# Performance work log

Measured on AMD Instinct MI355X. Metric: run time of the kernel, lower is better.

Reference implementation:

```python
import jax, jax.numpy as jnp
import numpy as np

N = 100000   # nodes of target type
N1 = 80000   # nodes of second type
D = 128      # raw feature dim
H = 64       # hidden dim
C = 16       # n_classes
G = 3        # number of graphs (metapaths)
E = 1000000  # edges per graph
K = 20       # neighbors per node for NS branch
LP_LAYERS = 3


def setup_inputs() -> dict:
    key = jax.random.key(0)
    ks = jax.random.split(key, 24)
    f = lambda i, shape: jax.random.normal(ks[i], shape, dtype=jnp.float32)
    feats0 = f(0, (N, D))
    feats1 = f(1, (N1, D))
    W0 = f(2, (D, H)) * 0.05
    b0 = jnp.zeros((H,), jnp.float32)
    W1 = f(3, (D, H)) * 0.05
    b1 = jnp.zeros((H,), jnp.float32)
    Wp = f(4, (D, H)) * 0.05
    Wcls = f(5, (H, C)) * 0.05
    bcls = jnp.zeros((C,), jnp.float32)
    alpha = f(6, (N, 1)) * 0.1
    attention = f(7, (N, G, 1))
    y = jax.random.randint(ks[8], (N,), 0, C)
    labels_one_hot = jax.nn.one_hot(y, C, dtype=jnp.float32)
    byte_idx_train = jax.random.bernoulli(ks[9], 0.3, (N, 1))
    label_init = jnp.full((N, C), 1.0 / C, jnp.float32)
    nei_idx = jax.random.randint(ks[10], (N, K), 0, N1, dtype=jnp.int32)
    src0 = jax.random.randint(ks[11], (E,), 0, N, dtype=jnp.int32)
    dst0 = jax.random.randint(ks[12], (E,), 0, N, dtype=jnp.int32)
    src1 = jax.random.randint(ks[13], (E,), 0, N, dtype=jnp.int32)
    dst1 = jax.random.randint(ks[14], (E,), 0, N, dtype=jnp.int32)
    src2 = jax.random.randint(ks[15], (E,), 0, N, dtype=jnp.int32)
    dst2 = jax.random.randint(ks[16], (E,), 0, N, dtype=jnp.int32)
    return dict(feats0=feats0, feats1=feats1, W0=W0, b0=b0, W1=W1, b1=b1,
                Wp=Wp, Wcls=Wcls, bcls=bcls, alpha=alpha, attention=attention,
                labels_one_hot=labels_one_hot, label_init=label_init,
                byte_idx_train=byte_idx_train, nei_idx=nei_idx,
                src0=src0, dst0=dst0, src1=src1, dst1=dst1, src2=src2, dst2=dst2)


def _propagate(fp, h, src, dst, n):
    # edge attention: dot-product score of projected feats, softmax per dst
    s = jnp.sum(fp[src] * fp[dst], axis=-1) / np.sqrt(fp.shape[-1])   # [E]
    m = jax.ops.segment_max(s, dst, num_segments=n)                   # [N]
    e = jnp.exp(s - jnp.where(jnp.isfinite(m), m, 0.0)[dst])          # [E]
    denom = jax.ops.segment_sum(e, dst, num_segments=n)               # [N]
    att = e / (denom[dst] + 1e-16)                                    # [E]
    return jax.ops.segment_sum(att[:, None] * h[src], dst, num_segments=n)


def reference(feats0, feats1, W0, b0, W1, b1, Wp, Wcls, bcls, alpha, attention,
              labels_one_hot, label_init, byte_idx_train, nei_idx,
              src0, dst0, src1, dst1, src2, dst2):
    n = label_init.shape[0]
    masked = byte_idx_train.astype(jnp.float32)          # [N,1]
    masked_label = 1.0 - masked                          # (~mask).float()
    masked_onehot = labels_one_hot * masked              # clamp train labels

    fp = feats0 @ Wp                                     # shared projected feats [N,H]
    h_prime = []
    for src, dst in ((src0, dst0), (src1, dst1), (src2, dst2)):
        h = label_init
        for _ in range(LP_LAYERS):
            h = _propagate(fp, h, src, dst, n)
            h = h * masked_label + masked_onehot
        h_prime.append(h)
    x = jnp.stack(h_prime, axis=-1)                      # [N, C, G]
    att_g = jax.nn.softmax(attention, axis=1)            # [N, G, 1]
    logits_lp = jnp.matmul(x, att_g).squeeze(-1)         # [N, C]

    # NS_ec branch: per-type projection + neighbor-mean aggregation + classifier
    h0 = feats0 @ W0 + b0                                # [N, H]
    h1 = feats1 @ W1 + b1                                # [N1, H]
    z = h0 + jnp.mean(h1[nei_idx], axis=1)               # [N, H]
    logits_ns = z @ Wcls + bcls                          # [N, C]

    gate = jax.nn.sigmoid(alpha)
    logits = gate * logits_lp + jax.nn.sigmoid(-alpha) * logits_ns
    return logits, logits_lp, logits_ns
```

## Files before the change

### kernel.cpp

```cpp
#include <hip/hip_runtime.h>
#include <stdint.h>
#include <stddef.h>

__device__ __forceinline__ float bl(unsigned u){ return __uint_as_float(u << 16); }
__device__ __forceinline__ float bh(unsigned u){ return __uint_as_float(u & 0xffff0000u); }
__device__ __forceinline__ unsigned short f2bf(float f){
    unsigned u = __float_as_uint(f);
    unsigned r = (u + 0x7fffu + ((u >> 16) & 1u)) >> 16;
    return (unsigned short)r;
}
__device__ __forceinline__ void ntstore_u2(uint2* p, unsigned x, unsigned y){
    unsigned long long v = ((unsigned long long)y << 32) | (unsigned long long)x;
    __builtin_nontemporal_store(v, (unsigned long long*)p);
}
__device__ __forceinline__ float get_mask(const void* p, unsigned flags, int i){
    if((flags & 1u) == 0) return ((const int*)p)[i] ? 1.0f : 0.0f;
    if(flags & 2u)        return ((const float*)p)[i];
    return ((const unsigned char*)p)[i] ? 1.0f : 0.0f;
}

__global__ __launch_bounds__(256) void prep_kernel(
    const float* __restrict__ W0, const float* __restrict__ b0,
    const float* __restrict__ W1, const float* __restrict__ b1,
    const float* __restrict__ Wcls, const float* __restrict__ bcls,
    float* __restrict__ W0c, float* __restrict__ W1c,
    float* __restrict__ b0c, float* __restrict__ b1c,
    const unsigned char* __restrict__ mp, int n,
    const unsigned* __restrict__ li, long li_n, unsigned* __restrict__ flags,
    int* __restrict__ deg, int n3)
{
    int t = threadIdx.x;
    if(blockIdx.x == 0){
        for(int i = t; i < 2048; i += 256){
            int d = i >> 4, c = i & 15;
            float s0 = 0.f, s1 = 0.f;
            for(int k = 0; k < 64; k++){
                float wc = Wcls[k*16 + c];
                s0 += W0[d*64 + k]*wc;
                s1 += W1[d*64 + k]*wc;
            }
            W0c[i] = s0; W1c[i] = s1;
        }
        if(t < 16){
            float s0 = 0.f, s1 = 0.f;
            for(int k = 0; k < 64; k++){
                float wc = Wcls[k*16 + t];
                s0 += b0[k]*wc; s1 += b1[k]*wc;
            }
            b0c[t] = s0 + bcls[t];
            b1c[t] = s1;
        }
    } else {
        long i = (long)(blockIdx.x - 1)*256 + t;
        if(i < n3) deg[i] = 0;
        unsigned f = 0;
        if(i < n){
            unsigned char b = mp[i];
            if((i & 3) && b) f |= 1u;
            if(b == 0x3Fu)   f |= 2u;
        }
        if(i < li_n){
            if(li[i] != li[0]) f |= 4u;
        }
        if(f) atomicOr(flags, f);
    }
}

__global__ __launch_bounds__(256) void proj_fused0(
    const float* __restrict__ X, const float* __restrict__ Wp,
    const float* __restrict__ W0c, const float* __restrict__ b0c,
    unsigned short* __restrict__ fph, float* __restrict__ h0c, int rows)
{
    __shared__ float Wl[128*64];
    __shared__ float Wcl[128*16];
    __shared__ float ftile[32*128];
    int t = threadIdx.x;
    for(int i = t; i < 2048; i += 256) ((float4*)Wl)[i]  = ((const float4*)Wp)[i];
    for(int i = t; i < 512;  i += 256) ((float4*)Wcl)[i] = ((const float4*)W0c)[i];
    int c4 = (t & 15)*4;
    int col16 = t & 15;
    int r2 = (t >> 4)*2;
    float bc = b0c[col16];
    for(long base = (long)blockIdx.x*32; base < rows; base += (long)gridDim.x*32){
        int nr = min(32, (int)(rows - base));
        __syncthreads();
        for(int i = t; i < nr*32; i += 256){
            int r = i >> 5, q = i & 31;
            ((float4*)ftile)[r*32 + q] = ((const float4*)X)[(base + r)*32 + q];
        }
        __syncthreads();
        float a00=0,a01=0,a02=0,a03=0, a10=0,a11=0,a12=0,a13=0;
        float c0 = bc, c1 = bc;
        #pragma unroll 4
        for(int k = 0; k < 128; k++){
            float4 w = *((const float4*)(Wl + k*64 + c4));
            float wc = Wcl[k*16 + col16];
            float x0 = ftile[r2*128 + k];
            float x1 = ftile[(r2+1)*128 + k];
            a00 += x0*w.x; a01 += x0*w.y; a02 += x0*w.z; a03 += x0*w.w; c0 += x0*wc;
            a10 += x1*w.x; a11 += x1*w.y; a12 += x1*w.z; a13 += x1*w.w; c1 += x1*wc;
        }
        if(r2 < nr){
            ushort4 o; o.x=f2bf(a00); o.y=f2bf(a01); o.z=f2bf(a02); o.w=f2bf(a03);
            *((ushort4*)(fph + (base + r2)*64 + c4)) = o;
            h0c[(base + r2)*16 + col16] = c0;
        }
        if(r2 + 1 < nr){
            ushort4 o; o.x=f2bf(a10); o.y=f2bf(a11); o.z=f2bf(a12); o.w=f2bf(a13);
            *((ushort4*)(fph + (base + r2 + 1)*64 + c4)) = o;
            h0c[(base + r2 + 1)*16 + col16] = c1;
        }
    }
}

__global__ __launch_bounds__(256) void proj16_count_kernel(
    const float* __restrict__ X, const float* __restrict__ Wc,
    const float* __restrict__ biasc, unsigned short* __restrict__ Y, int rows,
    int nbProj,
    const int* __restrict__ dst0, const int* __restrict__ dst1, const int* __restrict__ dst2,
    int* __restrict__ deg, int n, int eg)
{
    __shared__ float Wcl[128*16];
    __shared__ float ftile[64*128];
    int t = threadIdx.x;
    if(blockIdx.x < nbProj){
        for(int i = t; i < 512; i += 256) ((float4*)Wcl)[i] = ((const float4*)Wc)[i];
        int col = t & 15;
        int r4 = (t >> 4)*4;
        float bc = biasc[col];
        long base = (long)blockIdx.x*64;
        if(base < rows){
            int nr = min(64, (int)(rows - base));
            __syncthreads();
            for(int i = t; i < nr*32; i += 256){
                int r = i >> 5, q = i & 31;
                ((float4*)ftile)[r*32 + q] = ((const float4*)X)[(base + r)*32 + q];
            }
            __syncthreads();
            float acc0 = bc, acc1 = bc, acc2 = bc, acc3 = bc;
            #pragma unroll 4
            for(int k = 0; k < 128; k++){
                float wc = Wcl[k*16 + col];
                acc0 += ftile[(r4+0)*128 + k]*wc;
                acc1 += ftile[(r4+1)*128 + k]*wc;
                acc2 += ftile[(r4+2)*128 + k]*wc;
                acc3 += ftile[(r4+3)*128 + k]*wc;
            }
            if(r4+0 < nr) Y[(base + r4 + 0)*16 + col] = f2bf(acc0);
            if(r4+1 < nr) Y[(base + r4 + 1)*16 + col] = f2bf(acc1);
            if(r4+2 < nr) Y[(base + r4 + 2)*16 + col] = f2bf(acc2);
            if(r4+3 < nr) Y[(base + r4 + 3)*16 + col] = f2bf(acc3);
        }
    } else {
        long tid = (long)(blockIdx.x - nbProj)*256 + t;
        if(tid < 3L*eg){
            int g = (int)(tid / eg);
            int e = (int)(tid - (long)g*eg);
            const int* dp = g==0 ? dst0 : (g==1 ? dst1 : dst2);
            atomicAdd(&deg[(long)g*n + dp[e]], 1);
        }
    }
}

__global__ __launch_bounds__(256) void scanA_kernel(const int* __restrict__ deg,
                                                    int* __restrict__ incl,
                                                    int* __restrict__ bsum, int n3)
{
    __shared__ int sh[256];
    int t = threadIdx.x;
    long base = (long)blockIdx.x*1024 + t*4;
    int v0=0,v1=0,v2=0,v3=0;
    if(base   < n3) v0 = deg[base];
    if(base+1 < n3) v1 = deg[base+1];
    if(base+2 < n3) v2 = deg[base+2];
    if(base+3 < n3) v3 = deg[base+3];
    int tot = v0+v1+v2+v3;
    sh[t] = tot;
    __syncthreads();
    for(int ofs = 1; ofs < 256; ofs <<= 1){
        int add = (t >= ofs) ? sh[t-ofs] : 0;
        __syncthreads();
        sh[t] += add;
        __syncthreads();
    }
    int pre = sh[t] - tot;
    if(t == 255) bsum[blockIdx.x] = sh[255];
    int s0 = pre+v0, s1 = s0+v1, s2 = s1+v2, s3 = s2+v3;
    if(base   < n3) incl[base]   = s0;
    if(base+1 < n3) incl[base+1] = s1;
    if(base+2 < n3) incl[base+2] = s2;
    if(base+3 < n3) incl[base+3] = s3;
}

__global__ __launch_bounds__(512) void scanB_kernel(int* __restrict__ bsum, int nb)
{
    __shared__ int sh[512];
    int t = threadIdx.x;
    int v = (t < nb) ? bsum[t] : 0;
    sh[t] = v;
    __syncthreads();
    for(int ofs = 1; ofs < 512; ofs <<= 1){
        int add = (t >= ofs) ? sh[t-ofs] : 0;
        __syncthreads();
        sh[t] += add;
        __syncthreads();
    }
    if(t < nb) bsum[t] = sh[t] - v;
}

__global__ __launch_bounds__(256) void scanC_kernel(
    const int* __restrict__ incl, const int* __restrict__ boff,
    int* __restrict__ rowptr, int* __restrict__ cursor, int n3,
    const float* __restrict__ label_init, const float* __restrict__ labels,
    const void* __restrict__ maskp, const unsigned* __restrict__ flags,
    unsigned short* __restrict__ hA, int n)
{
    int i = blockIdx.x*blockDim.x + threadIdx.x;
    if(i >= n3) return;
    int ex = (i == 0) ? 0 : (incl[i-1] + boff[(i-1) >> 10]);
    int en = incl[i] + boff[i >> 10];
    rowptr[i] = ex;
    cursor[i] = ex;
    if(i == n3-1) rowptr[n3] = en;
    unsigned fl = *flags;
    if(!(fl & 4u)){
        int g = i / n;
        int d = i - g*n;
        float mk = get_mask(maskp, fl, d);
        float v = (en > ex) ? label_init[0]*(1.0f - mk) : 0.0f;
        const float4* lb = (const float4*)(labels + (long)d*16);
        ushort4* op = (ushort4*)(hA + (long)i*16);
        #pragma unroll
        for(int q = 0; q < 4; q++){
            float4 l4 = lb[q];
            ushort4 o;
            o.x = f2bf(v + l4.x*mk);
            o.y = f2bf(v + l4.y*mk);
            o.z = f2bf(v + l4.z*mk);
            o.w = f2bf(v + l4.w*mk);
            op[q] = o;
        }
    }
}

__global__ __launch_bounds__(256) void score_scatter_packed(
    const unsigned short* __restrict__ fph,
    const int* __restrict__ src0, const int* __restrict__ dst0,
    const int* __restrict__ src1, const int* __restrict__ dst1,
    const int* __restrict__ src2, const int* __restrict__ dst2,
    int* __restrict__ cursor, uint2* __restrict__ rec, int n, int eg)
{
    long tid = (long)blockIdx.x*blockDim.x + threadIdx.x;
    long gid = tid >> 3;
    long tot = 3L*eg;
    long e0 = gid*4;
    if(e0 >= tot) return;
    int l = threadIdx.x & 7;
    const uint4* f4 = (const uint4*)fph;

    int sv[4], dv[4], gv[4];
    bool ok[4];
    #pragma unroll
    for(int q = 0; q < 4; q++){
        long e = e0 + q;
        ok[q] = (e < tot);
        long ee = ok[q] ? e : (tot - 1);
        int g = (int)(ee / eg);
        int i = (int)(ee - (long)g*eg);
        const int* sp = g==0 ? src0 : (g==1 ? src1 : src2);
        const int* dp = g==0 ? dst0 : (g==1 ? dst1 : dst2);
        sv[q] = sp[i];
        dv[q] = dp[i];
        gv[q] = g;
    }
    uint4 A[4], B[4];
    #pragma unroll
    for(int q = 0; q < 4; q++){
        A[q] = f4[(long)sv[q]*8 + l];
        B[q] = f4[(long)dv[q]*8 + l];
    }
    float p[4];
    #pragma unroll
    for(int q = 0; q < 4; q++){
        float v;
        v  = bl(A[q].x)*bl(B[q].x) + bh(A[q].x)*bh(B[q].x);
        v += bl(A[q].y)*bl(B[q].y) + bh(A[q].y)*bh(B[q].y);
        v += bl(A[q].z)*bl(B[q].z) + bh(A[q].z)*bh(B[q].z);
        v += bl(A[q].w)*bl(B[q].w) + bh(A[q].w)*bh(B[q].w);
        p[q] = v;
    }
    #pragma unroll
    for(int q = 0; q < 4; q++){
        p[q] += __shfl_xor(p[q], 1);
        p[q] += __shfl_xor(p[q], 2);
        p[q] += __shfl_xor(p[q], 4);
    }
    if(l == 0){
        int pos[4];
        #pragma unroll
        for(int q = 0; q < 4; q++){
            if(ok[q]) pos[q] = atomicAdd(&cursor[(long)gv[q]*n + dv[q]], 1);
        }
        #pragma unroll
        for(int q = 0; q < 4; q++){
            if(ok[q]){
                float ev = __expf(fminf(p[q]*0.125f, 70.0f));
                ntstore_u2(&rec[pos[q]], (unsigned)sv[q], __float_as_uint(ev));
            }
        }
    }
}

__device__ __forceinline__ void prop_row_bf16(
    const uint2* __restrict__ rec, int beg, int end,
    const unsigned short* __restrict__ hg, int c4,
    float &a0, float &a1, float &a2, float &a3)
{
    float den = 0.f;
    a0 = a1 = a2 = a3 = 0.f;
    int j = beg;
    if((j & 1) && j < end){
        uint2 r = rec[j];
        float e = __uint_as_float(r.y);
        den += e;
        uint2 hv = *((const uint2*)(hg + (long)r.x*16 + c4));
        a0 += e*bl(hv.x); a1 += e*bh(hv.x); a2 += e*bl(hv.y); a3 += e*bh(hv.y);
        j++;
    }
    for(; j + 1 < end; j += 2){
        uint4 rr = *((const uint4*)(&rec[j]));
        float e0 = __uint_as_float(rr.y);
        float e1 = __uint_as_float(rr.w);
        den += e0 + e1;
        uint2 hv0 = *((const uint2*)(hg + (long)rr.x*16 + c4));
        uint2 hv1 = *((const uint2*)(hg + (long)rr.z*16 + c4));
        a0 += e0*bl(hv0.x) + e1*bl(hv1.x);
        a1 += e0*bh(hv0.x) + e1*bh(hv1.x);
        a2 += e0*bl(hv0.y) + e1*bl(hv1.y);
        a3 += e0*bh(hv0.y) + e1*bh(hv1.y);
    }
    if(j < end){
        uint2 r = rec[j];
        float e = __uint_as_float(r.y);
        den += e;
        uint2 hv = *((const uint2*)(hg + (long)r.x*16 + c4));
        a0 += e*bl(hv.x); a1 += e*bh(hv.x); a2 += e*bl(hv.y); a3 += e*bh(hv.y);
    }
    float inv = 1.0f/(den + 1e-16f);
    a0 *= inv; a1 *= inv; a2 *= inv; a3 *= inv;
}

__global__ __launch_bounds__(256) void prop1_fallback_kernel(
    const int* __restrict__ rowptr, const uint2* __restrict__ rec,
    const float* __restrict__ h_in_f32, unsigned short* __restrict__ h_next,
    const float* __restrict__ labels, const void* __restrict__ maskp,
    const unsigned* __restrict__ flags, int n)
{
    unsigned fl = *flags;
    if(!(fl & 4u)) return;
    long tid = (long)blockIdx.x*blockDim.x + threadIdx.x;
    int row = (int)(tid >> 2);
    int c4 = (int)(tid & 3)*4;
    if(row >= 3*n) return;
    int g = row / n;
    int d = row - g*n;
    int beg = rowptr[row], end = rowptr[row+1];
    float a0=0.f, a1=0.f, a2=0.f, a3=0.f, den=0.f;
    for(int j = beg; j < end; j++){
        uint2 r = rec[j];
        float e = __uint_as_float(r.y);
        den += e;
        float4 hv = *((const float4*)(h_in_f32 + (long)r.x*16 + c4));
        a0 += e*hv.x; a1 += e*hv.y; a2 += e*hv.z; a3 += e*hv.w;
    }
    float inv = 1.0f/(den + 1e-16f);
    float mk = get_mask(maskp, fl, d);
    float im = (1.0f - mk)*inv;
    float4 lb = *((const float4*)(labels + (long)d*16 + c4));
    ushort4 o;
    o.x = f2bf(a0*im + lb.x*mk);
    o.y = f2bf(a1*im + lb.y*mk);
    o.z = f2bf(a2*im + lb.z*mk);
    o.w = f2bf(a3*im + lb.w*mk);
    *((ushort4*)(h_next + (long)row*16 + c4)) = o;
}

__global__ __launch_bounds__(256) void prop_mid_kernel(
    const int* __restrict__ rowptr, const uint2* __restrict__ rec,
    const unsigned short* __restrict__ h_in, unsigned short* __restrict__ h_next,
    const float* __restrict__ labels, const void* __restrict__ maskp,
    const unsigned* __restrict__ flags, int n)
{
    long tid = (long)blockIdx.x*blockDim.x + threadIdx.x;
    int row = (int)(tid >> 2);
    int c4 = (int)(tid & 3)*4;
    if(row >= 3*n) return;
    int g = row / n;
    int d = row - g*n;
    float a0, a1, a2, a3;
    prop_row_bf16(rec, rowptr[row], rowptr[row+1], h_in + (long)g*n*16, c4,
                  a0, a1, a2, a3);
    unsigned fl = *flags;
    float mk = get_mask(maskp, fl, d);
    float im = 1.0f - mk;
    float4 lb = *((const float4*)(labels + (long)d*16 + c4));
    ushort4 o;
    o.x = f2bf(a0*im + lb.x*mk);
    o.y = f2bf(a1*im + lb.y*mk);
    o.z = f2bf(a2*im + lb.z*mk);
    o.w = f2bf(a3*im + lb.w*mk);
    *((ushort4*)(h_next + (long)row*16 + c4)) = o;
}

__global__ __launch_bounds__(256) void prop3_ns_kernel(
    const int* __restrict__ rowptr, const uint2* __restrict__ rec,
    const unsigned short* __restrict__ h_in, const float* __restrict__ labels,
    const void* __restrict__ maskp, const unsigned* __restrict__ flags,
    const float* __restrict__ h0c, const unsigned short* __restrict__ h1c,
    const int* __restrict__ nei, const float* __restrict__ attn,
    const float* __restrict__ alpha, float* __restrict__ out, int n, int kk)
{
    long tid = (long)blockIdx.x*blockDim.x + threadIdx.x;
    int node = (int)(tid >> 2);
    int c4 = (int)(tid & 3)*4;
    if(node >= n) return;
    unsigned fl = *flags;
    float mk = get_mask(maskp, fl, node);
    float im = 1.0f - mk;
    float4 lb = *((const float4*)(labels + (long)node*16 + c4));

    float lp_[3][4];
    #pragma unroll
    for(int g = 0; g < 3; g++){
        int row = g*n + node;
        float a0, a1, a2, a3;
        prop_row_bf16(rec, rowptr[row], rowptr[row+1], h_in + (long)g*n*16, c4,
                      a0, a1, a2, a3);
        lp_[g][0] = a0*im + lb.x*mk;
        lp_[g][1] = a1*im + lb.y*mk;
        lp_[g][2] = a2*im + lb.z*mk;
        lp_[g][3] = a3*im + lb.w*mk;
    }
    float t0 = attn[node*3], t1 = attn[node*3+1], t2 = attn[node*3+2];
    float mx = fmaxf(t0, fmaxf(t1, t2));
    float e0 = __expf(t0-mx), e1 = __expf(t1-mx), e2 = __expf(t2-mx);
    float inv = 1.0f/(e0+e1+e2);
    e0 *= inv; e1 *= inv; e2 *= inv;
    float lp0 = e0*lp_[0][0] + e1*lp_[1][0] + e2*lp_[2][0];
    float lp1 = e0*lp_[0][1] + e1*lp_[1][1] + e2*lp_[2][1];
    float lp2 = e0*lp_[0][2] + e1*lp_[1][2] + e2*lp_[2][2];
    float lp3 = e0*lp_[0][3] + e1*lp_[1][3] + e2*lp_[2][3];

    const int* nrow = nei + (long)node*kk;
    float s0=0.f, s1=0.f, s2=0.f, s3=0.f;
    for(int j = 0; j < kk; j++){
        int nb = nrow[j];
        uint2 hv = *((const uint2*)(h1c + (long)nb*16 + c4));
        s0 += bl(hv.x); s1 += bh(hv.x); s2 += bl(hv.y); s3 += bh(hv.y);
    }
    float invk = 1.0f/(float)kk;
    float4 h0 = *((const float4*)(h0c + (long)node*16 + c4));
    float ns0 = h0.x + s0*invk, ns1 = h0.y + s1*invk;
    float ns2 = h0.z + s2*invk, ns3 = h0.w + s3*invk;

    float al = alpha[node];
    float sg = 1.0f/(1.0f + __expf(-al));
    float isg = 1.0f - sg;
    long gs = (long)n*16;
    long idx = (long)node*16 + c4;
    float4 o0; o0.x = sg*lp0 + isg*ns0; o0.y = sg*lp1 + isg*ns1;
               o0.z = sg*lp2 + isg*ns2; o0.w = sg*lp3 + isg*ns3;
    float4 o1; o1.x = lp0; o1.y = lp1; o1.z = lp2; o1.w = lp3;
    float4 o2; o2.x = ns0; o2.y = ns1; o2.z = ns2; o2.w = ns3;
    *((float4*)(out + idx))        = o0;
    *((float4*)(out + gs + idx))   = o1;
    *((float4*)(out + 2*gs + idx)) = o2;
}

extern "C" void kernel_launch(void* const* d_in, const int* in_sizes, int n_in,
                              void* d_out, int out_size, void* d_ws, size_t ws_size,
                              hipStream_t stream)
{
    const float* feats0     = (const float*)d_in[0];
    const float* feats1     = (const float*)d_in[1];
    const float* W0         = (const float*)d_in[2];
    const float* b0         = (const float*)d_in[3];
    const float* W1         = (const float*)d_in[4];
    const float* b1         = (const float*)d_in[5];
    const float* Wp         = (const float*)d_in[6];
    const float* Wcls       = (const float*)d_in[7];
    const float* bcls       = (const float*)d_in[8];
    const float* alpha      = (const float*)d_in[9];
    const float* attn       = (const float*)d_in[10];
    const float* labels     = (const float*)d_in[11];
    const float* label_init = (const float*)d_in[12];
    const void*  maskp      = d_in[13];
    const int*   nei        = (const int*)d_in[14];
    const int*   src0       = (const int*)d_in[15];
    const int*   dst0       = (const int*)d_in[16];
    const int*   src1       = (const int*)d_in[17];
    const int*   dst1       = (const int*)d_in[18];
    const int*   src2       = (const int*)d_in[19];
    const int*   dst2       = (const int*)d_in[20];

    const int n  = in_sizes[9];
    const int n1 = in_sizes[1] / 128;
    const int eg = in_sizes[15];
    const int kk = in_sizes[14] / n;
    const int n3 = 3*n;

    char* ws = (char*)d_ws;
    size_t off = 0;
    auto alloc = [&](size_t bytes)->char*{
        char* p = ws + off; off += (bytes + 255) & ~(size_t)255; return p;
    };
    unsigned*       flags  = (unsigned*)      alloc(256);
    unsigned short* fph    = (unsigned short*)alloc((size_t)n*64*2);
    float*          h0c    = (float*)         alloc((size_t)n*16*4);
    unsigned short* h1c    = (unsigned short*)alloc((size_t)n1*16*2);
    float*          W0c    = (float*)         alloc(2048*4);
    float*          W1c    = (float*)         alloc(2048*4);
    float*          b0c    = (float*)         alloc(64);
    float*          b1c    = (float*)         alloc(64);
    int*            deg    = (int*)           alloc((size_t)n3*4);
    int*            cursor = (int*)           alloc((size_t)n3*4);
    int*            bsum   = (int*)           alloc(512*4);
    int*            rowptr = (int*)           alloc(((size_t)n3+1)*4);
    uint2*          rec    = (uint2*)         alloc((size_t)3*eg*8);
    unsigned short* hA     = (unsigned short*)alloc((size_t)n3*16*2);
    unsigned short* hB     = (unsigned short*)alloc((size_t)n3*16*2);
    int* incl = deg;

    hipMemsetAsync(flags, 0, 4, stream);

    long li_n = (long)n*16;
    {
        unsigned gsz = 1 + (unsigned)((li_n + 255)/256);
        prep_kernel<<<gsz, 256, 0, stream>>>(W0, b0, W1, b1, Wcls, bcls,
                                             W0c, W1c, b0c, b1c,
                                             (const unsigned char*)maskp, n,
                                             (const unsigned*)label_init, li_n, flags,
                                             deg, n3);
    }

    proj_fused0<<<(n+31)/32, 256, 0, stream>>>(feats0, Wp, W0c, b0c, fph, h0c, n);
    {
        int nbProj = (n1 + 63)/64;
        long tot = 3L*eg;
        unsigned nbCount = (unsigned)((tot + 255)/256);
        proj16_count_kernel<<<nbProj + nbCount, 256, 0, stream>>>(
            feats1, W1c, b1c, h1c, n1, nbProj, dst0, dst1, dst2, deg, n, eg);
    }

    int nb = (n3 + 1023)/1024;
    scanA_kernel<<<nb, 256, 0, stream>>>(deg, incl, bsum, n3);
    scanB_kernel<<<1, 512, 0, stream>>>(bsum, nb);
    scanC_kernel<<<(n3+255)/256, 256, 0, stream>>>(incl, bsum, rowptr, cursor, n3,
                                                   label_init, labels, maskp, flags,
                                                   hA, n);

    {
        long groups = (3L*eg + 3)/4;
        long tthreads = groups*8;
        score_scatter_packed<<<(unsigned)((tthreads+255)/256), 256, 0, stream>>>(
            fph, src0,dst0,src1,dst1,src2,dst2, cursor, rec, n, eg);
    }

    prop1_fallback_kernel<<<(unsigned)(((long)n3*4+255)/256), 256, 0, stream>>>(
        rowptr, rec, label_init, hA, labels, maskp, flags, n);
    prop_mid_kernel<<<(unsigned)(((long)n3*4+255)/256), 256, 0, stream>>>(
        rowptr, rec, hA, hB, labels, maskp, flags, n);

    prop3_ns_kernel<<<(unsigned)(((long)n*4+255)/256), 256, 0, stream>>>(
        rowptr, rec, hB, labels, maskp, flags, h0c, h1c, nei, attn, alpha,
        (float*)d_out, n, kk);
}
```

Measured before the change: 483.0 us.

## Pack edge records into 32 bits and move NS aggregation into mid propagation

Edge records shrink from 8 bytes (int src plus float exp score) to one 32-bit word holding a 17-bit source index and a 15-bit reduced-precision exponent value. The score is clamped to [-10, 10] before the exponent. This halves record traffic in the scatter and in all three propagation passes. The NS neighbor-mean branch now runs in extra blocks of the middle propagation kernel and writes logits_ns to the output, which the final kernel reads back. The risks are lower precision in the attention weights, a changed softmax from the clamp, and an assumption that node indices fit in 17 bits (n ≤ 131072).

```diff
diff --git a/kernel.cpp b/kernel.cpp
--- a/kernel.cpp
+++ b/kernel.cpp
@@ -9,9 +9,8 @@
     unsigned r = (u + 0x7fffu + ((u >> 16) & 1u)) >> 16;
     return (unsigned short)r;
 }
-__device__ __forceinline__ void ntstore_u2(uint2* p, unsigned x, unsigned y){
-    unsigned long long v = ((unsigned long long)y << 32) | (unsigned long long)x;
-    __builtin_nontemporal_store(v, (unsigned long long*)p);
+__device__ __forceinline__ float dec15(unsigned e15){
+    return __uint_as_float((e15 + (112u << 10)) << 13);
 }
 __device__ __forceinline__ float get_mask(const void* p, unsigned flags, int i){
     if((flags & 1u) == 0) return ((const int*)p)[i] ? 1.0f : 0.0f;
@@ -248,7 +247,7 @@
     const int* __restrict__ src0, const int* __restrict__ dst0,
     const int* __restrict__ src1, const int* __restrict__ dst1,
     const int* __restrict__ src2, const int* __restrict__ dst2,
-    int* __restrict__ cursor, uint2* __restrict__ rec, int n, int eg)
+    int* __restrict__ cursor, unsigned* __restrict__ rec, int n, int eg)
 {
     long tid = (long)blockIdx.x*blockDim.x + threadIdx.x;
     long gid = tid >> 3;
@@ -304,15 +303,18 @@
         #pragma unroll
         for(int q = 0; q < 4; q++){
             if(ok[q]){
-                float ev = __expf(fminf(p[q]*0.125f, 70.0f));
-                ntstore_u2(&rec[pos[q]], (unsigned)sv[q], __float_as_uint(ev));
+                float s = fminf(fmaxf(p[q]*0.125f, -10.0f), 10.0f);
+                unsigned u = __float_as_uint(__expf(s)) + 0x1000u;
+                unsigned e15 = (u >> 13) - (112u << 10);
+                unsigned pk = (e15 << 17) | (unsigned)sv[q];
+                __builtin_nontemporal_store(pk, rec + pos[q]);
             }
         }
     }
 }
 
 __device__ __forceinline__ void prop_row_bf16(
-    const uint2* __restrict__ rec, int beg, int end,
+    const unsigned* __restrict__ rec, int beg, int end,
     const unsigned short* __restrict__ hg, int c4,
     float &a0, float &a1, float &a2, float &a3)
 {
@@ -320,30 +322,30 @@
     a0 = a1 = a2 = a3 = 0.f;
     int j = beg;
     if((j & 1) && j < end){
-        uint2 r = rec[j];
-        float e = __uint_as_float(r.y);
+        unsigned p = rec[j];
+        float e = dec15(p >> 17);
         den += e;
-        uint2 hv = *((const uint2*)(hg + (long)r.x*16 + c4));
+        uint2 hv = *((const uint2*)(hg + (long)(p & 0x1FFFFu)*16 + c4));
         a0 += e*bl(hv.x); a1 += e*bh(hv.x); a2 += e*bl(hv.y); a3 += e*bh(hv.y);
         j++;
     }
     for(; j + 1 < end; j += 2){
-        uint4 rr = *((const uint4*)(&rec[j]));
-        float e0 = __uint_as_float(rr.y);
-        float e1 = __uint_as_float(rr.w);
+        uint2 rr = *((const uint2*)(rec + j));
+        float e0 = dec15(rr.x >> 17);
+        float e1 = dec15(rr.y >> 17);
         den += e0 + e1;
-        uint2 hv0 = *((const uint2*)(hg + (long)rr.x*16 + c4));
-        uint2 hv1 = *((const uint2*)(hg + (long)rr.z*16 + c4));
+        uint2 hv0 = *((const uint2*)(hg + (long)(rr.x & 0x1FFFFu)*16 + c4));
+        uint2 hv1 = *((const uint2*)(hg + (long)(rr.y & 0x1FFFFu)*16 + c4));
         a0 += e0*bl(hv0.x) + e1*bl(hv1.x);
         a1 += e0*bh(hv0.x) + e1*bh(hv1.x);
         a2 += e0*bl(hv0.y) + e1*bl(hv1.y);
         a3 += e0*bh(hv0.y) + e1*bh(hv1.y);
     }
     if(j < end){
-        uint2 r = rec[j];
-        float e = __uint_as_float(r.y);
+        unsigned p = rec[j];
+        float e = dec15(p >> 17);
         den += e;
-        uint2 hv = *((const uint2*)(hg + (long)r.x*16 + c4));
+        uint2 hv = *((const uint2*)(hg + (long)(p & 0x1FFFFu)*16 + c4));
         a0 += e*bl(hv.x); a1 += e*bh(hv.x); a2 += e*bl(hv.y); a3 += e*bh(hv.y);
     }
     float inv = 1.0f/(den + 1e-16f);
@@ -351,7 +353,7 @@
 }
 
 __global__ __launch_bounds__(256) void prop1_fallback_kernel(
-    const int* __restrict__ rowptr, const uint2* __restrict__ rec,
+    const int* __restrict__ rowptr, const unsigned* __restrict__ rec,
     const float* __restrict__ h_in_f32, unsigned short* __restrict__ h_next,
     const float* __restrict__ labels, const void* __restrict__ maskp,
     const unsigned* __restrict__ flags, int n)
@@ -367,10 +369,10 @@
     int beg = rowptr[row], end = rowptr[row+1];
     float a0=0.f, a1=0.f, a2=0.f, a3=0.f, den=0.f;
     for(int j = beg; j < end; j++){
-        uint2 r = rec[j];
-        float e = __uint_as_float(r.y);
+        unsigned p = rec[j];
+        float e = dec15(p >> 17);
         den += e;
-        float4 hv = *((const float4*)(h_in_f32 + (long)r.x*16 + c4));
+        float4 hv = *((const float4*)(h_in_f32 + (long)(p & 0x1FFFFu)*16 + c4));
         a0 += e*hv.x; a1 += e*hv.y; a2 += e*hv.z; a3 += e*hv.w;
     }
     float inv = 1.0f/(den + 1e-16f);
@@ -385,40 +387,62 @@
     *((ushort4*)(h_next + (long)row*16 + c4)) = o;
 }
 
-__global__ __launch_bounds__(256) void prop_mid_kernel(
-    const int* __restrict__ rowptr, const uint2* __restrict__ rec,
+__global__ __launch_bounds__(256) void prop_mid_ns_kernel(
+    const int* __restrict__ rowptr, const unsigned* __restrict__ rec,
     const unsigned short* __restrict__ h_in, unsigned short* __restrict__ h_next,
     const float* __restrict__ labels, const void* __restrict__ maskp,
-    const unsigned* __restrict__ flags, int n)
-{
-    long tid = (long)blockIdx.x*blockDim.x + threadIdx.x;
-    int row = (int)(tid >> 2);
-    int c4 = (int)(tid & 3)*4;
-    if(row >= 3*n) return;
-    int g = row / n;
-    int d = row - g*n;
-    float a0, a1, a2, a3;
-    prop_row_bf16(rec, rowptr[row], rowptr[row+1], h_in + (long)g*n*16, c4,
-                  a0, a1, a2, a3);
-    unsigned fl = *flags;
-    float mk = get_mask(maskp, fl, d);
-    float im = 1.0f - mk;
-    float4 lb = *((const float4*)(labels + (long)d*16 + c4));
-    ushort4 o;
-    o.x = f2bf(a0*im + lb.x*mk);
-    o.y = f2bf(a1*im + lb.y*mk);
-    o.z = f2bf(a2*im + lb.z*mk);
-    o.w = f2bf(a3*im + lb.w*mk);
-    *((ushort4*)(h_next + (long)row*16 + c4)) = o;
+    const unsigned* __restrict__ flags, int n, int nbMid,
+    const float* __restrict__ h0c, const unsigned short* __restrict__ h1c,
+    const int* __restrict__ nei, float* __restrict__ out, int kk)
+{
+    int t = threadIdx.x;
+    if(blockIdx.x < nbMid){
+        long tid = (long)blockIdx.x*256 + t;
+        int row = (int)(tid >> 2);
+        int c4 = (int)(tid & 3)*4;
+        if(row >= 3*n) return;
+        int g = row / n;
+        int d = row - g*n;
+        float a0, a1, a2, a3;
+        prop_row_bf16(rec, rowptr[row], rowptr[row+1], h_in + (long)g*n*16, c4,
+                      a0, a1, a2, a3);
+        unsigned fl = *flags;
+        float mk = get_mask(maskp, fl, d);
+        float im = 1.0f - mk;
+        float4 lb = *((const float4*)(labels + (long)d*16 + c4));
+        ushort4 o;
+        o.x = f2bf(a0*im + lb.x*mk);
+        o.y = f2bf(a1*im + lb.y*mk);
+        o.z = f2bf(a2*im + lb.z*mk);
+        o.w = f2bf(a3*im + lb.w*mk);
+        *((ushort4*)(h_next + (long)row*16 + c4)) = o;
+    } else {
+        long tid = (long)(blockIdx.x - nbMid)*256 + t;
+        int node = (int)(tid >> 2);
+        int c4 = (int)(tid & 3)*4;
+        if(node >= n) return;
+        const int* nrow = nei + (long)node*kk;
+        float s0=0.f, s1=0.f, s2=0.f, s3=0.f;
+        for(int j = 0; j < kk; j++){
+            int nb = nrow[j];
+            uint2 hv = *((const uint2*)(h1c + (long)nb*16 + c4));
+            s0 += bl(hv.x); s1 += bh(hv.x); s2 += bl(hv.y); s3 += bh(hv.y);
+        }
+        float invk = 1.0f/(float)kk;
+        float4 h0 = *((const float4*)(h0c + (long)node*16 + c4));
+        float4 o2;
+        o2.x = h0.x + s0*invk; o2.y = h0.y + s1*invk;
+        o2.z = h0.z + s2*invk; o2.w = h0.w + s3*invk;
+        *((float4*)(out + (long)2*n*16 + (long)node*16 + c4)) = o2;
+    }
 }
 
 __global__ __launch_bounds__(256) void prop3_ns_kernel(
-    const int* __restrict__ rowptr, const uint2* __restrict__ rec,
+    const int* __restrict__ rowptr, const unsigned* __restrict__ rec,
     const unsigned short* __restrict__ h_in, const float* __restrict__ labels,
     const void* __restrict__ maskp, const unsigned* __restrict__ flags,
-    const float* __restrict__ h0c, const unsigned short* __restrict__ h1c,
-    const int* __restrict__ nei, const float* __restrict__ attn,
-    const float* __restrict__ alpha, float* __restrict__ out, int n, int kk)
+    const float* __restrict__ attn, const float* __restrict__ alpha,
+    float* __restrict__ out, int n)
 {
     long tid = (long)blockIdx.x*blockDim.x + threadIdx.x;
     int node = (int)(tid >> 2);
@@ -451,30 +475,17 @@
     float lp2 = e0*lp_[0][2] + e1*lp_[1][2] + e2*lp_[2][2];
     float lp3 = e0*lp_[0][3] + e1*lp_[1][3] + e2*lp_[2][3];
 
-    const int* nrow = nei + (long)node*kk;
-    float s0=0.f, s1=0.f, s2=0.f, s3=0.f;
-    for(int j = 0; j < kk; j++){
-        int nb = nrow[j];
-        uint2 hv = *((const uint2*)(h1c + (long)nb*16 + c4));
-        s0 += bl(hv.x); s1 += bh(hv.x); s2 += bl(hv.y); s3 += bh(hv.y);
-    }
-    float invk = 1.0f/(float)kk;
-    float4 h0 = *((const float4*)(h0c + (long)node*16 + c4));
-    float ns0 = h0.x + s0*invk, ns1 = h0.y + s1*invk;
-    float ns2 = h0.z + s2*invk, ns3 = h0.w + s3*invk;
-
+    long gs = (long)n*16;
+    long idx = (long)node*16 + c4;
+    float4 ns = *((const float4*)(out + 2*gs + idx));
     float al = alpha[node];
     float sg = 1.0f/(1.0f + __expf(-al));
     float isg = 1.0f - sg;
-    long gs = (long)n*16;
-    long idx = (long)node*16 + c4;
-    float4 o0; o0.x = sg*lp0 + isg*ns0; o0.y = sg*lp1 + isg*ns1;
-               o0.z = sg*lp2 + isg*ns2; o0.w = sg*lp3 + isg*ns3;
+    float4 o0; o0.x = sg*lp0 + isg*ns.x; o0.y = sg*lp1 + isg*ns.y;
+               o0.z = sg*lp2 + isg*ns.z; o0.w = sg*lp3 + isg*ns.w;
     float4 o1; o1.x = lp0; o1.y = lp1; o1.z = lp2; o1.w = lp3;
-    float4 o2; o2.x = ns0; o2.y = ns1; o2.z = ns2; o2.w = ns3;
-    *((float4*)(out + idx))        = o0;
-    *((float4*)(out + gs + idx))   = o1;
-    *((float4*)(out + 2*gs + idx)) = o2;
+    *((float4*)(out + idx))      = o0;
+    *((float4*)(out + gs + idx)) = o1;
 }
 
 extern "C" void kernel_launch(void* const* d_in, const int* in_sizes, int n_in,
@@ -526,7 +537,7 @@
     int*            cursor = (int*)           alloc((size_t)n3*4);
     int*            bsum   = (int*)           alloc(512*4);
     int*            rowptr = (int*)           alloc(((size_t)n3+1)*4);
-    uint2*          rec    = (uint2*)         alloc((size_t)3*eg*8);
+    unsigned*       rec    = (unsigned*)      alloc((size_t)3*eg*4);
     unsigned short* hA     = (unsigned short*)alloc((size_t)n3*16*2);
     unsigned short* hB     = (unsigned short*)alloc((size_t)n3*16*2);
     int* incl = deg;
@@ -568,10 +579,14 @@
 
     prop1_fallback_kernel<<<(unsigned)(((long)n3*4+255)/256), 256, 0, stream>>>(
         rowptr, rec, label_init, hA, labels, maskp, flags, n);
-    prop_mid_kernel<<<(unsigned)(((long)n3*4+255)/256), 256, 0, stream>>>(
-        rowptr, rec, hA, hB, labels, maskp, flags, n);
+    {
+        int nbMid = (int)(((long)n3*4 + 255)/256);
+        int nbNS  = (int)(((long)n*4 + 255)/256);
+        prop_mid_ns_kernel<<<nbMid + nbNS, 256, 0, stream>>>(
+            rowptr, rec, hA, hB, labels, maskp, flags, n, nbMid,
+            h0c, h1c, nei, (float*)d_out, kk);
+    }
 
     prop3_ns_kernel<<<(unsigned)(((long)n*4+255)/256), 256, 0, stream>>>(
-        rowptr, rec, hB, labels, maskp, flags, h0c, h1c, nei, attn, alpha,
-        (float*)d_out, n, kk);
-}
+        rowptr, rec, hB, labels, maskp, flags, attn, alpha, (float*)d_out, n);
+}
```

Measured after the change: 477.5 us. No clear change (-1.2%).
